# Optimization experiments

Measured on AMD Instinct MI355X. Metric: run time of the kernel, lower is better.

Reference implementation:

```python
import jax, jax.numpy as jnp
import numpy as np

B, T, C = 4, 2048, 1024
L = 256
H = 16
HS = C // H  # 64

def setup_inputs() -> dict:
    key = jax.random.key(0)
    ks = jax.random.split(key, 6)
    s = 0.02
    return {
        "x": jax.random.normal(ks[0], (B, T, C), dtype=jnp.float32),
        "Wq": jax.random.normal(ks[1], (C, C), dtype=jnp.float32) * s,
        "W_kv_down": jax.random.normal(ks[2], (C, L), dtype=jnp.float32) * s,
        "W_k_up": jax.random.normal(ks[3], (L, C), dtype=jnp.float32) * s,
        "W_v_up": jax.random.normal(ks[4], (L, C), dtype=jnp.float32) * s,
        "W_out": jax.random.normal(ks[5], (C, C), dtype=jnp.float32) * s,
    }

def reference(x, Wq, W_kv_down, W_k_up, W_v_up, W_out):
    # x: [B,T,C]
    q = (x @ Wq).reshape(B, T, H, HS).transpose(0, 2, 1, 3)        # [B,H,T,HS]
    latent_kv = x @ W_kv_down                                       # [B,T,L]
    k = (latent_kv @ W_k_up).reshape(B, T, H, HS).transpose(0, 2, 1, 3)
    v = (latent_kv @ W_v_up).reshape(B, T, H, HS).transpose(0, 2, 1, 3)
    att = jnp.einsum('bhtd,bhsd->bhts', q, k) / jnp.sqrt(jnp.float32(HS))
    causal = jnp.tril(jnp.ones((T, T), dtype=bool))
    att = jnp.where(causal[None, None], att, jnp.float32(-jnp.inf))
    att = jax.nn.softmax(att, axis=-1)
    y = jnp.einsum('bhts,bhsd->bhtd', att, v)                       # [B,H,T,HS]
    y = y.transpose(0, 2, 1, 3).reshape(B, T, C)
    return y @ W_out
```

## Files before the change

kernel.cpp:

```cpp
#include <hip/hip_runtime.h>
#include <cstddef>
#include <cstdint>

#define BB 4
#define TT 2048
#define CC 1024
#define LL 256
#define HH 16
#define DD 64
#define QLD (CC + LL)

typedef __attribute__((ext_vector_type(8))) short s16x8;
typedef __attribute__((ext_vector_type(4))) float f32x4;

static __device__ inline unsigned short f2bf(float f) {
    union { float f; unsigned u; } v; v.f = f;
    unsigned r = v.u + 0x7fffu + ((v.u >> 16) & 1u);
    return (unsigned short)(r >> 16);
}

static __device__ inline float fast_exp2(float x) {
#if __has_builtin(__builtin_amdgcn_exp2f)
    return __builtin_amdgcn_exp2f(x);
#else
    return exp2f(x);
#endif
}

static __device__ inline unsigned pack_bf16_trunc(float lo, float hi) {
    union { float f; unsigned u; } a, b;
    a.f = lo; b.f = hi;
    return __builtin_amdgcn_perm(b.u, a.u, 0x07060302u);
}

#define GLDS16(g, l)                                             \
    __builtin_amdgcn_global_load_lds(                            \
        (__attribute__((address_space(1))) void*)(g),            \
        (__attribute__((address_space(3))) void*)(l), 16, 0, 0)

extern "C" __global__ __launch_bounds__(256)
void fused_cvt(const float* __restrict__ x, unsigned short* __restrict__ xb,
               const float* __restrict__ Wq, const float* __restrict__ Wkv,
               const float* __restrict__ Wk, const float* __restrict__ Wv,
               const float* __restrict__ Wo,
               unsigned short* __restrict__ W1t, unsigned short* __restrict__ W2t,
               unsigned short* __restrict__ Wot, float qscale) {
    __shared__ unsigned short Ts[64][72];
    const int t = threadIdx.x;
    int blk = blockIdx.x;
    if (blk < 8192) {
        const int i = blk * 256 + t;
        const float4 v = ((const float4*)x)[i];
        ushort4 o;
        o.x = f2bf(v.x); o.y = f2bf(v.y); o.z = f2bf(v.z); o.w = f2bf(v.w);
        ((ushort4*)xb)[i] = o;
        return;
    }
    blk -= 8192;
    const float* W; unsigned short* Wt; int K, N; float scale; int tile;
    if (blk < 256)      { W = Wq;  Wt = W1t;                      K = CC; N = CC; scale = qscale; tile = blk; }
    else if (blk < 320) { W = Wkv; Wt = W1t + (size_t)CC * CC;    K = CC; N = LL; scale = 1.f;    tile = blk - 256; }
    else if (blk < 384) { W = Wk;  Wt = W2t;                      K = LL; N = CC; scale = 1.f;    tile = blk - 320; }
    else if (blk < 448) { W = Wv;  Wt = W2t + (size_t)CC * LL;    K = LL; N = CC; scale = 1.f;    tile = blk - 384; }
    else                { W = Wo;  Wt = Wot;                      K = CC; N = CC; scale = 1.f;    tile = blk - 448; }
    const int ktiles = K >> 6;
    const int k0 = (tile % ktiles) * 64, n0 = (tile / ktiles) * 64;
#pragma unroll
    for (int l = 0; l < 4; ++l) {
        const int idx = t + l * 256;
        const int r = idx >> 4, c4 = (idx & 15) * 4;
        const float4 v = *(const float4*)(W + (size_t)(k0 + r) * N + n0 + c4);
        Ts[c4 + 0][r] = f2bf(v.x * scale); Ts[c4 + 1][r] = f2bf(v.y * scale);
        Ts[c4 + 2][r] = f2bf(v.z * scale); Ts[c4 + 3][r] = f2bf(v.w * scale);
    }
    __syncthreads();
#pragma unroll
    for (int l = 0; l < 2; ++l) {
        const int idx = t + l * 256;
        const int n = idx >> 3, seg = idx & 7;
        *(s16x8*)(Wt + (size_t)(n0 + n) * K + k0 + seg * 8) = *(const s16x8*)&Ts[n][seg * 8];
    }
}

template <int MODE>
__global__ __launch_bounds__(256)
void bgemm(const unsigned short* __restrict__ A, const unsigned short* __restrict__ Bt,
           void* __restrict__ Cv, void* __restrict__ Cv2,
           int M, int N, int K, int lda, int ldc) {
    __shared__ unsigned short As[128][64];
    __shared__ unsigned short Bs[128][64];
    const int t = threadIdx.x;
    const int w = t >> 6, lane = t & 63, quad = lane >> 4, l16 = lane & 15;
    const int wm = w & 1, wn = w >> 1;

    int wg = blockIdx.y * gridDim.x + blockIdx.x;
    const int nwg = gridDim.x * gridDim.y;
    if ((nwg & 7) == 0) wg = (wg & 7) * (nwg >> 3) + (wg >> 3);
    const int bx = wg % gridDim.x, by = wg / gridDim.x;
    const int row0 = by * 128, col0 = bx * 128;

    const int sr = lane >> 3;
    const int sc = ((lane & 7) ^ sr) * 8;

    f32x4 acc[4][4];
#pragma unroll
    for (int i = 0; i < 4; ++i)
#pragma unroll
        for (int j = 0; j < 4; ++j) acc[i][j] = (f32x4){0.f, 0.f, 0.f, 0.f};

    const unsigned short* Ab = A + (size_t)(row0 + w * 32 + sr) * lda + sc;
    const unsigned short* Bb = Bt + (size_t)(col0 + w * 32 + sr) * K + sc;

    for (int k0 = 0; k0 < K; k0 += 64) {
#pragma unroll
        for (int c = 0; c < 4; ++c) {
            GLDS16(Ab + (size_t)(c * 8) * lda + k0, &As[w * 32 + c * 8][0]);
            GLDS16(Bb + (size_t)(c * 8) * K + k0, &Bs[w * 32 + c * 8][0]);
        }
        __syncthreads();
#pragma unroll
        for (int kk = 0; kk < 2; ++kk) {
            s16x8 af[4], bfr[4];
#pragma unroll
            for (int mt = 0; mt < 4; ++mt)
                af[mt] = *(const s16x8*)
                    &As[wm * 64 + mt * 16 + l16][((kk * 4 + quad) ^ (l16 & 7)) * 8];
#pragma unroll
            for (int nt = 0; nt < 4; ++nt)
                bfr[nt] = *(const s16x8*)
                    &Bs[wn * 64 + nt * 16 + l16][((kk * 4 + quad) ^ (l16 & 7)) * 8];
#pragma unroll
            for (int mt = 0; mt < 4; ++mt)
#pragma unroll
                for (int nt = 0; nt < 4; ++nt)
                    acc[mt][nt] = __builtin_amdgcn_mfma_f32_16x16x32_bf16(
                        af[mt], bfr[nt], acc[mt][nt], 0, 0, 0);
        }
        __syncthreads();
    }

    if constexpr (MODE == 0) {
        float* C = (float*)Cv;
#pragma unroll
        for (int mt = 0; mt < 4; ++mt)
#pragma unroll
            for (int nt = 0; nt < 4; ++nt)
#pragma unroll
                for (int r = 0; r < 4; ++r)
                    C[(size_t)(row0 + wm * 64 + mt * 16 + quad * 4 + r) * ldc +
                      col0 + wn * 64 + nt * 16 + l16] = acc[mt][nt][r];
    } else if constexpr (MODE == 1) {
        unsigned short* C = (unsigned short*)Cv;
#pragma unroll
        for (int mt = 0; mt < 4; ++mt)
#pragma unroll
            for (int nt = 0; nt < 4; ++nt)
#pragma unroll
                for (int r = 0; r < 4; ++r)
                    C[(size_t)(row0 + wm * 64 + mt * 16 + quad * 4 + r) * ldc +
                      col0 + wn * 64 + nt * 16 + l16] = f2bf(acc[mt][nt][r]);
    } else {
        if (col0 < CC) {
            unsigned short* C = (unsigned short*)Cv;
#pragma unroll
            for (int mt = 0; mt < 4; ++mt)
#pragma unroll
                for (int nt = 0; nt < 4; ++nt)
#pragma unroll
                    for (int r = 0; r < 4; ++r)
                        C[(size_t)(row0 + wm * 64 + mt * 16 + quad * 4 + r) * ldc +
                          col0 + wn * 64 + nt * 16 + l16] = f2bf(acc[mt][nt][r]);
        } else {
            __shared__ unsigned short Tb[64][136];
            unsigned short* vt = (unsigned short*)Cv2;
            const int b   = row0 >> 11;
            const int tl0 = row0 & 2047;
#pragma unroll
            for (int h = 0; h < 2; ++h) {
                if (wn == h) {
#pragma unroll
                    for (int mt = 0; mt < 4; ++mt)
#pragma unroll
                        for (int nt = 0; nt < 4; ++nt)
#pragma unroll
                            for (int r = 0; r < 4; ++r)
                                Tb[nt * 16 + l16][wm * 64 + mt * 16 + quad * 4 + r] =
                                    f2bf(acc[mt][nt][r]);
                }
                __syncthreads();
                const int head = ((col0 - CC) >> 6) + h;
#pragma unroll
                for (int l = 0; l < 4; ++l) {
                    const int idx = t + l * 256;
                    const int dv = idx >> 4, seg = idx & 15;
                    *(s16x8*)(vt + (((size_t)b * HH + head) * DD + dv) * TT + tl0 + seg * 8) =
                        *(const s16x8*)&Tb[dv][seg * 8];
                }
                __syncthreads();
            }
        }
    }
}

extern "C" __global__ __launch_bounds__(256, 4)
void mla_attn2(const unsigned short* __restrict__ q,
               const unsigned short* __restrict__ k,
               const unsigned short* __restrict__ vt,
               unsigned short* __restrict__ y) {
    __shared__ unsigned short Ks[2][64][64];
    __shared__ unsigned short Vs[2][64][64];

    {
        const unsigned bid = blockIdx.y * gridDim.x + blockIdx.x;
        const unsigned stag = (bid * 0x9E3779B1u) >> 30;
        for (unsigned i = 0; i < stag; ++i) __builtin_amdgcn_s_sleep(23);
    }

    const int bh = blockIdx.x;
    const int qt2 = (gridDim.y - 1) - blockIdx.y;
    const int b = bh >> 4, h = bh & 15;
    const int t0 = qt2 * 128;
    const int t = threadIdx.x;
    const int w = t >> 6, lane = t & 63, quad = lane >> 4, l16 = lane & 15;
    const int qw0 = t0 + w * 32;
    const int swz = ((lane & 7) ^ ((lane >> 3) & 7)) * 8;
    const int lrow = lane >> 3;

    const unsigned short* kb0 = k + ((size_t)b * TT) * CC + h * DD;
    const unsigned short* vb0 = vt + ((size_t)(b * HH + h)) * DD * TT;

    s16x8 qf[2][2];
#pragma unroll
    for (int qs = 0; qs < 2; ++qs)
#pragma unroll
        for (int kh = 0; kh < 2; ++kh)
            qf[qs][kh] = *(const s16x8*)(q + ((size_t)b * TT + qw0 + qs * 16 + l16) * QLD +
                                         h * DD + kh * 32 + quad * 8);

    f32x4 o[2][4];
    float lsum[2] = {0.f, 0.f};
#pragma unroll
    for (int qs = 0; qs < 2; ++qs)
#pragma unroll
        for (int nt = 0; nt < 4; ++nt) o[qs][nt] = (f32x4){0.f, 0.f, 0.f, 0.f};

    const int nkt = 2 * qt2 + 2;

#define STAGE_KV(kt_, bi_)                                                     \
    do {                                                                       \
        const int s0_ = (kt_) * 64;                                            \
        _Pragma("unroll")                                                      \
        for (int c = 0; c < 2; ++c) {                                          \
            const int g = w * 2 + c;                                           \
            const int row = g * 8 + lrow;                                      \
            GLDS16(kb0 + (size_t)(s0_ + row) * CC + swz, &Ks[bi_][g * 8][0]);  \
            GLDS16(vb0 + (size_t)row * TT + s0_ + swz, &Vs[bi_][g * 8][0]);    \
        }                                                                      \
    } while (0)

    STAGE_KV(0, 0);
    __syncthreads();

    for (int kt = 0; kt < nkt; ++kt) {
        const int cur = kt & 1;
        if (kt + 1 < nkt) STAGE_KV(kt + 1, cur ^ 1);

        const int s0 = kt * 64;
        if (s0 <= qw0 + 31) {
            const unsigned short (*Kc)[64] = Ks[cur];
            const unsigned short (*Vc)[64] = Vs[cur];
            f32x4 st[2][4];
#pragma unroll
            for (int nt = 0; nt < 4; ++nt) {
                const int key = nt * 16 + l16;
                const s16x8 kf0 = *(const s16x8*)&Kc[key][((0 + quad) ^ (l16 & 7)) * 8];
                const s16x8 kf1 = *(const s16x8*)&Kc[key][((4 + quad) ^ (l16 & 7)) * 8];
#pragma unroll
                for (int qs = 0; qs < 2; ++qs) {
                    f32x4 acc = (f32x4){0.f, 0.f, 0.f, 0.f};
                    acc = __builtin_amdgcn_mfma_f32_16x16x32_bf16(kf0, qf[qs][0], acc, 0, 0, 0);
                    acc = __builtin_amdgcn_mfma_f32_16x16x32_bf16(kf1, qf[qs][1], acc, 0, 0, 0);
                    st[qs][nt] = acc;
                }
            }

            const bool maskedTile = (s0 + 63 > qw0);
            s16x8 pf[2][2];
#pragma unroll
            for (int qs = 0; qs < 2; ++qs) {
                const int qidx = qw0 + qs * 16 + l16;
                unsigned pc[4][2];
                float tsum = 0.f;
#pragma unroll
                for (int nt = 0; nt < 4; ++nt) {
                    const int key0 = s0 + nt * 16 + quad * 4;
                    float p[4];
#pragma unroll
                    for (int r = 0; r < 4; ++r) {
                        float sv = st[qs][nt][r];
                        if (maskedTile && (key0 + r > qidx)) sv = -1e30f;
                        p[r] = fast_exp2(sv);
                    }
                    tsum += (p[0] + p[1]) + (p[2] + p[3]);
                    pc[nt][0] = pack_bf16_trunc(p[0], p[1]);
                    pc[nt][1] = pack_bf16_trunc(p[2], p[3]);
                }
                lsum[qs] += tsum;
#pragma unroll
                for (int kh = 0; kh < 2; ++kh) {
                    auto s0a = __builtin_amdgcn_permlane32_swap(
                        (int)pc[2 * kh + 0][0], (int)pc[2 * kh + 1][0], false, false);
                    auto w02 = __builtin_amdgcn_permlane16_swap(s0a[0], s0a[1], false, false);
                    auto s1a = __builtin_amdgcn_permlane32_swap(
                        (int)pc[2 * kh + 0][1], (int)pc[2 * kh + 1][1], false, false);
                    auto w13 = __builtin_amdgcn_permlane16_swap(s1a[0], s1a[1], false, false);
                    union { unsigned u[4]; s16x8 v; } fu;
                    fu.u[0] = (unsigned)w02[0];
                    fu.u[1] = (unsigned)w13[0];
                    fu.u[2] = (unsigned)w02[1];
                    fu.u[3] = (unsigned)w13[1];
                    pf[qs][kh] = fu.v;
                }
            }

#pragma unroll
            for (int nt = 0; nt < 4; ++nt) {
                const int dv = nt * 16 + l16;
                const s16x8 vf0 = *(const s16x8*)&Vc[dv][((0 + quad) ^ (l16 & 7)) * 8];
                const s16x8 vf1 = *(const s16x8*)&Vc[dv][((4 + quad) ^ (l16 & 7)) * 8];
#pragma unroll
                for (int qs = 0; qs < 2; ++qs) {
                    o[qs][nt] = __builtin_amdgcn_mfma_f32_16x16x32_bf16(pf[qs][0], vf0,
                                                                        o[qs][nt], 0, 0, 0);
                    o[qs][nt] = __builtin_amdgcn_mfma_f32_16x16x32_bf16(pf[qs][1], vf1,
                                                                        o[qs][nt], 0, 0, 0);
                }
            }
        }
        __syncthreads();
    }

    float lfull[2];
#pragma unroll
    for (int qs = 0; qs < 2; ++qs) {
        float s = lsum[qs];
        s += __shfl_xor(s, 16);
        s += __shfl_xor(s, 32);
        lfull[qs] = s;
    }

#pragma unroll
    for (int qs = 0; qs < 2; ++qs) {
#pragma unroll
        for (int r = 0; r < 4; ++r) {
            const float inv = 1.f / __shfl(lfull[qs], quad * 4 + r);
            unsigned short* yb = y + ((size_t)b * TT + qw0 + qs * 16 + quad * 4 + r) * CC +
                                 h * DD + l16;
#pragma unroll
            for (int nt = 0; nt < 4; ++nt)
                yb[nt * 16] = f2bf(o[qs][nt][r] * inv);
        }
    }
}

extern "C" void kernel_launch(void* const* d_in, const int* in_sizes, int n_in,
                              void* d_out, int out_size, void* d_ws, size_t ws_size,
                              hipStream_t stream) {
    const float* x   = (const float*)d_in[0];
    const float* Wq  = (const float*)d_in[1];
    const float* Wkv = (const float*)d_in[2];
    const float* Wk  = (const float*)d_in[3];
    const float* Wv  = (const float*)d_in[4];
    const float* Wo  = (const float*)d_in[5];
    float* out = (float*)d_out;

    const int M = BB * TT;
    unsigned short* p = (unsigned short*)d_ws;
    unsigned short* xb    = p; p += (size_t)M * CC;
    unsigned short* qlatb = p; p += (size_t)M * QLD;
    unsigned short* kb    = p; p += (size_t)M * CC;
    unsigned short* vtb   = p; p += (size_t)M * CC;
    unsigned short* yb    = p; p += (size_t)M * CC;
    unsigned short* W1t   = p; p += (size_t)QLD * CC;
    unsigned short* W2t   = p; p += (size_t)(2 * CC) * LL;
    unsigned short* Wot   = p; p += (size_t)CC * CC;

    const float qscale = 0.125f * 1.44269504f;

    fused_cvt<<<8896, 256, 0, stream>>>(x, xb, Wq, Wkv, Wk, Wv, Wo,
                                        W1t, W2t, Wot, qscale);
    bgemm<1><<<dim3(QLD / 128, M / 128), 256, 0, stream>>>(
        xb, W1t, qlatb, nullptr, M, QLD, CC, CC, QLD);
    bgemm<3><<<dim3(2 * CC / 128, M / 128), 256, 0, stream>>>(
        qlatb + CC, W2t, kb, vtb, M, 2 * CC, LL, QLD, CC);
    mla_attn2<<<dim3(BB * HH, TT / 128), 256, 0, stream>>>(qlatb, kb, vtb, yb);
    bgemm<0><<<dim3(CC / 128, M / 128), 256, 0, stream>>>(
        yb, Wot, out, nullptr, M, CC, CC, CC, CC);
}
```

Before: 227.6 us.

## Pair complementary causal query tiles per block for balanced attention work

The attention kernel now uses 128-thread blocks, each handling two 64-row query tiles (qt = 31-p and qt = p), so every block does roughly the same amount of causal work. Previously each block handled one 128-row tile with four waves, and the blocks' causal work varied widely. Each wave now stages twice as many K/V rows. The grid shrinks to 16 blocks per head, and each block runs its two tiles one after the other, so there is less parallelism per block and more load-issue work per thread.

```diff
diff --git a/kernel.cpp b/kernel.cpp
--- a/kernel.cpp
+++ b/kernel.cpp
@@ -202,8 +202,8 @@
     }
 }
 
-extern "C" __global__ __launch_bounds__(256, 4)
-void mla_attn2(const unsigned short* __restrict__ q,
+extern "C" __global__ __launch_bounds__(128, 2)
+void mla_attn4(const unsigned short* __restrict__ q,
                const unsigned short* __restrict__ k,
                const unsigned short* __restrict__ vt,
                unsigned short* __restrict__ y) {
@@ -217,148 +217,152 @@
     }
 
     const int bh = blockIdx.x;
-    const int qt2 = (gridDim.y - 1) - blockIdx.y;
     const int b = bh >> 4, h = bh & 15;
-    const int t0 = qt2 * 128;
     const int t = threadIdx.x;
     const int w = t >> 6, lane = t & 63, quad = lane >> 4, l16 = lane & 15;
-    const int qw0 = t0 + w * 32;
     const int swz = ((lane & 7) ^ ((lane >> 3) & 7)) * 8;
     const int lrow = lane >> 3;
+    const int p = blockIdx.y;
 
     const unsigned short* kb0 = k + ((size_t)b * TT) * CC + h * DD;
     const unsigned short* vb0 = vt + ((size_t)(b * HH + h)) * DD * TT;
 
-    s16x8 qf[2][2];
-#pragma unroll
-    for (int qs = 0; qs < 2; ++qs)
-#pragma unroll
-        for (int kh = 0; kh < 2; ++kh)
-            qf[qs][kh] = *(const s16x8*)(q + ((size_t)b * TT + qw0 + qs * 16 + l16) * QLD +
-                                         h * DD + kh * 32 + quad * 8);
-
-    f32x4 o[2][4];
-    float lsum[2] = {0.f, 0.f};
-#pragma unroll
-    for (int qs = 0; qs < 2; ++qs)
-#pragma unroll
-        for (int nt = 0; nt < 4; ++nt) o[qs][nt] = (f32x4){0.f, 0.f, 0.f, 0.f};
-
-    const int nkt = 2 * qt2 + 2;
-
-#define STAGE_KV(kt_, bi_)                                                     \
+#define STAGE_KV(s0_, bi_)                                                     \
     do {                                                                       \
-        const int s0_ = (kt_) * 64;                                            \
         _Pragma("unroll")                                                      \
-        for (int c = 0; c < 2; ++c) {                                          \
-            const int g = w * 2 + c;                                           \
+        for (int c = 0; c < 4; ++c) {                                          \
+            const int g = w * 4 + c;                                           \
             const int row = g * 8 + lrow;                                      \
-            GLDS16(kb0 + (size_t)(s0_ + row) * CC + swz, &Ks[bi_][g * 8][0]);  \
-            GLDS16(vb0 + (size_t)row * TT + s0_ + swz, &Vs[bi_][g * 8][0]);    \
+            GLDS16(kb0 + (size_t)((s0_) + row) * CC + swz, &Ks[bi_][g * 8][0]);\
+            GLDS16(vb0 + (size_t)row * TT + (s0_) + swz, &Vs[bi_][g * 8][0]);  \
         }                                                                      \
     } while (0)
 
-    STAGE_KV(0, 0);
-    __syncthreads();
-
-    for (int kt = 0; kt < nkt; ++kt) {
-        const int cur = kt & 1;
-        if (kt + 1 < nkt) STAGE_KV(kt + 1, cur ^ 1);
-
-        const int s0 = kt * 64;
-        if (s0 <= qw0 + 31) {
-            const unsigned short (*Kc)[64] = Ks[cur];
-            const unsigned short (*Vc)[64] = Vs[cur];
-            f32x4 st[2][4];
-#pragma unroll
-            for (int nt = 0; nt < 4; ++nt) {
-                const int key = nt * 16 + l16;
-                const s16x8 kf0 = *(const s16x8*)&Kc[key][((0 + quad) ^ (l16 & 7)) * 8];
-                const s16x8 kf1 = *(const s16x8*)&Kc[key][((4 + quad) ^ (l16 & 7)) * 8];
+#pragma unroll 1
+    for (int item = 0; item < 2; ++item) {
+        const int qt = item == 0 ? (31 - p) : p;
+        const int qw0 = qt * 64 + w * 32;
+
+        s16x8 qf[2][2];
+#pragma unroll
+        for (int qs = 0; qs < 2; ++qs)
+#pragma unroll
+            for (int kh = 0; kh < 2; ++kh)
+                qf[qs][kh] = *(const s16x8*)(q + ((size_t)b * TT + qw0 + qs * 16 + l16) * QLD +
+                                             h * DD + kh * 32 + quad * 8);
+
+        f32x4 o[2][4];
+        float lsum[2] = {0.f, 0.f};
+#pragma unroll
+        for (int qs = 0; qs < 2; ++qs)
+#pragma unroll
+            for (int nt = 0; nt < 4; ++nt) o[qs][nt] = (f32x4){0.f, 0.f, 0.f, 0.f};
+
+        const int nkt = qt + 1;
+
+        STAGE_KV(0, 0);
+        __syncthreads();
+
+#pragma unroll 1
+        for (int kt = 0; kt < nkt; ++kt) {
+            const int cur = kt & 1;
+            if (kt + 1 < nkt) STAGE_KV((kt + 1) * 64, cur ^ 1);
+
+            const int s0 = kt * 64;
+            if (s0 <= qw0 + 31) {
+                const unsigned short (*Kc)[64] = Ks[cur];
+                const unsigned short (*Vc)[64] = Vs[cur];
+                f32x4 st[2][4];
+#pragma unroll
+                for (int nt = 0; nt < 4; ++nt) {
+                    const int key = nt * 16 + l16;
+                    const s16x8 kf0 = *(const s16x8*)&Kc[key][((0 + quad) ^ (l16 & 7)) * 8];
+                    const s16x8 kf1 = *(const s16x8*)&Kc[key][((4 + quad) ^ (l16 & 7)) * 8];
+#pragma unroll
+                    for (int qs = 0; qs < 2; ++qs) {
+                        f32x4 acc = (f32x4){0.f, 0.f, 0.f, 0.f};
+                        acc = __builtin_amdgcn_mfma_f32_16x16x32_bf16(kf0, qf[qs][0], acc, 0, 0, 0);
+                        acc = __builtin_amdgcn_mfma_f32_16x16x32_bf16(kf1, qf[qs][1], acc, 0, 0, 0);
+                        st[qs][nt] = acc;
+                    }
+                }
+
+                const bool maskedTile = (s0 + 63 > qw0);
+                s16x8 pf[2][2];
 #pragma unroll
                 for (int qs = 0; qs < 2; ++qs) {
-                    f32x4 acc = (f32x4){0.f, 0.f, 0.f, 0.f};
-                    acc = __builtin_amdgcn_mfma_f32_16x16x32_bf16(kf0, qf[qs][0], acc, 0, 0, 0);
-                    acc = __builtin_amdgcn_mfma_f32_16x16x32_bf16(kf1, qf[qs][1], acc, 0, 0, 0);
-                    st[qs][nt] = acc;
+                    const int qidx = qw0 + qs * 16 + l16;
+                    unsigned pc[4][2];
+                    float tsum = 0.f;
+#pragma unroll
+                    for (int nt = 0; nt < 4; ++nt) {
+                        const int key0 = s0 + nt * 16 + quad * 4;
+                        float pv[4];
+#pragma unroll
+                        for (int r = 0; r < 4; ++r) {
+                            float sv = st[qs][nt][r];
+                            if (maskedTile && (key0 + r > qidx)) sv = -1e30f;
+                            pv[r] = fast_exp2(sv);
+                        }
+                        tsum += (pv[0] + pv[1]) + (pv[2] + pv[3]);
+                        pc[nt][0] = pack_bf16_trunc(pv[0], pv[1]);
+                        pc[nt][1] = pack_bf16_trunc(pv[2], pv[3]);
+                    }
+                    lsum[qs] += tsum;
+#pragma unroll
+                    for (int kh = 0; kh < 2; ++kh) {
+                        auto s0a = __builtin_amdgcn_permlane32_swap(
+                            (int)pc[2 * kh + 0][0], (int)pc[2 * kh + 1][0], false, false);
+                        auto w02 = __builtin_amdgcn_permlane16_swap(s0a[0], s0a[1], false, false);
+                        auto s1a = __builtin_amdgcn_permlane32_swap(
+                            (int)pc[2 * kh + 0][1], (int)pc[2 * kh + 1][1], false, false);
+                        auto w13 = __builtin_amdgcn_permlane16_swap(s1a[0], s1a[1], false, false);
+                        union { unsigned u[4]; s16x8 v; } fu;
+                        fu.u[0] = (unsigned)w02[0];
+                        fu.u[1] = (unsigned)w13[0];
+                        fu.u[2] = (unsigned)w02[1];
+                        fu.u[3] = (unsigned)w13[1];
+                        pf[qs][kh] = fu.v;
+                    }
+                }
+
+#pragma unroll
+                for (int nt = 0; nt < 4; ++nt) {
+                    const int dv = nt * 16 + l16;
+                    const s16x8 vf0 = *(const s16x8*)&Vc[dv][((0 + quad) ^ (l16 & 7)) * 8];
+                    const s16x8 vf1 = *(const s16x8*)&Vc[dv][((4 + quad) ^ (l16 & 7)) * 8];
+#pragma unroll
+                    for (int qs = 0; qs < 2; ++qs) {
+                        o[qs][nt] = __builtin_amdgcn_mfma_f32_16x16x32_bf16(pf[qs][0], vf0,
+                                                                            o[qs][nt], 0, 0, 0);
+                        o[qs][nt] = __builtin_amdgcn_mfma_f32_16x16x32_bf16(pf[qs][1], vf1,
+                                                                            o[qs][nt], 0, 0, 0);
+                    }
                 }
             }
-
-            const bool maskedTile = (s0 + 63 > qw0);
-            s16x8 pf[2][2];
-#pragma unroll
-            for (int qs = 0; qs < 2; ++qs) {
-                const int qidx = qw0 + qs * 16 + l16;
-                unsigned pc[4][2];
-                float tsum = 0.f;
-#pragma unroll
-                for (int nt = 0; nt < 4; ++nt) {
-                    const int key0 = s0 + nt * 16 + quad * 4;
-                    float p[4];
-#pragma unroll
-                    for (int r = 0; r < 4; ++r) {
-                        float sv = st[qs][nt][r];
-                        if (maskedTile && (key0 + r > qidx)) sv = -1e30f;
-                        p[r] = fast_exp2(sv);
-                    }
-                    tsum += (p[0] + p[1]) + (p[2] + p[3]);
-                    pc[nt][0] = pack_bf16_trunc(p[0], p[1]);
-                    pc[nt][1] = pack_bf16_trunc(p[2], p[3]);
-                }
-                lsum[qs] += tsum;
-#pragma unroll
-                for (int kh = 0; kh < 2; ++kh) {
-                    auto s0a = __builtin_amdgcn_permlane32_swap(
-                        (int)pc[2 * kh + 0][0], (int)pc[2 * kh + 1][0], false, false);
-                    auto w02 = __builtin_amdgcn_permlane16_swap(s0a[0], s0a[1], false, false);
-                    auto s1a = __builtin_amdgcn_permlane32_swap(
-                        (int)pc[2 * kh + 0][1], (int)pc[2 * kh + 1][1], false, false);
-                    auto w13 = __builtin_amdgcn_permlane16_swap(s1a[0], s1a[1], false, false);
-                    union { unsigned u[4]; s16x8 v; } fu;
-                    fu.u[0] = (unsigned)w02[0];
-                    fu.u[1] = (unsigned)w13[0];
-                    fu.u[2] = (unsigned)w02[1];
-                    fu.u[3] = (unsigned)w13[1];
-                    pf[qs][kh] = fu.v;
-                }
+            __syncthreads();
+        }
+
+        float lfull[2];
+#pragma unroll
+        for (int qs = 0; qs < 2; ++qs) {
+            float s = lsum[qs];
+            s += __shfl_xor(s, 16);
+            s += __shfl_xor(s, 32);
+            lfull[qs] = s;
+        }
+
+#pragma unroll
+        for (int qs = 0; qs < 2; ++qs) {
+#pragma unroll
+            for (int r = 0; r < 4; ++r) {
+                const float inv = 1.f / __shfl(lfull[qs], quad * 4 + r);
+                unsigned short* yb = y + ((size_t)b * TT + qw0 + qs * 16 + quad * 4 + r) * CC +
+                                     h * DD + l16;
+#pragma unroll
+                for (int nt = 0; nt < 4; ++nt)
+                    yb[nt * 16] = f2bf(o[qs][nt][r] * inv);
             }
-
-#pragma unroll
-            for (int nt = 0; nt < 4; ++nt) {
-                const int dv = nt * 16 + l16;
-                const s16x8 vf0 = *(const s16x8*)&Vc[dv][((0 + quad) ^ (l16 & 7)) * 8];
-                const s16x8 vf1 = *(const s16x8*)&Vc[dv][((4 + quad) ^ (l16 & 7)) * 8];
-#pragma unroll
-                for (int qs = 0; qs < 2; ++qs) {
-                    o[qs][nt] = __builtin_amdgcn_mfma_f32_16x16x32_bf16(pf[qs][0], vf0,
-                                                                        o[qs][nt], 0, 0, 0);
-                    o[qs][nt] = __builtin_amdgcn_mfma_f32_16x16x32_bf16(pf[qs][1], vf1,
-                                                                        o[qs][nt], 0, 0, 0);
-                }
-            }
-        }
-        __syncthreads();
-    }
-
-    float lfull[2];
-#pragma unroll
-    for (int qs = 0; qs < 2; ++qs) {
-        float s = lsum[qs];
-        s += __shfl_xor(s, 16);
-        s += __shfl_xor(s, 32);
-        lfull[qs] = s;
-    }
-
-#pragma unroll
-    for (int qs = 0; qs < 2; ++qs) {
-#pragma unroll
-        for (int r = 0; r < 4; ++r) {
-            const float inv = 1.f / __shfl(lfull[qs], quad * 4 + r);
-            unsigned short* yb = y + ((size_t)b * TT + qw0 + qs * 16 + quad * 4 + r) * CC +
-                                 h * DD + l16;
-#pragma unroll
-            for (int nt = 0; nt < 4; ++nt)
-                yb[nt * 16] = f2bf(o[qs][nt][r] * inv);
         }
     }
 }
@@ -393,7 +397,7 @@
         xb, W1t, qlatb, nullptr, M, QLD, CC, CC, QLD);
     bgemm<3><<<dim3(2 * CC / 128, M / 128), 256, 0, stream>>>(
         qlatb + CC, W2t, kb, vtb, M, 2 * CC, LL, QLD, CC);
-    mla_attn2<<<dim3(BB * HH, TT / 128), 256, 0, stream>>>(qlatb, kb, vtb, yb);
+    mla_attn4<<<dim3(BB * HH, 16), 128, 0, stream>>>(qlatb, kb, vtb, yb);
     bgemm<0><<<dim3(CC / 128, M / 128), 256, 0, stream>>>(
         yb, Wot, out, nullptr, M, CC, CC, CC, CC);
 }
```

New measurement: 242.1 us. +6.4%, slower.

## Drop K/V double buffering in attention kernel and raise occupancy hint

Applied to the files above, without the earlier changes.

Removes the double-buffered shared-memory staging of K and V tiles in the attention kernel and uses a single buffer that is loaded and then synchronized each iteration. The launch bounds hint moves from 4 to 8 blocks per SM, halving LDS use per block so more waves can be resident. In exchange, the prefetch overlap of the next tile with compute is lost, and each tile load is now exposed, to be hidden only by the extra occupancy.

```diff
diff --git a/kernel.cpp b/kernel.cpp
--- a/kernel.cpp
+++ b/kernel.cpp
@@ -202,13 +202,13 @@
     }
 }
 
-extern "C" __global__ __launch_bounds__(256, 4)
+extern "C" __global__ __launch_bounds__(256, 8)
 void mla_attn2(const unsigned short* __restrict__ q,
                const unsigned short* __restrict__ k,
                const unsigned short* __restrict__ vt,
                unsigned short* __restrict__ y) {
-    __shared__ unsigned short Ks[2][64][64];
-    __shared__ unsigned short Vs[2][64][64];
+    __shared__ unsigned short Ks[64][64];
+    __shared__ unsigned short Vs[64][64];
 
     {
         const unsigned bid = blockIdx.y * gridDim.x + blockIdx.x;
@@ -246,35 +246,24 @@
 
     const int nkt = 2 * qt2 + 2;
 
-#define STAGE_KV(kt_, bi_)                                                     \
-    do {                                                                       \
-        const int s0_ = (kt_) * 64;                                            \
-        _Pragma("unroll")                                                      \
-        for (int c = 0; c < 2; ++c) {                                          \
-            const int g = w * 2 + c;                                           \
-            const int row = g * 8 + lrow;                                      \
-            GLDS16(kb0 + (size_t)(s0_ + row) * CC + swz, &Ks[bi_][g * 8][0]);  \
-            GLDS16(vb0 + (size_t)row * TT + s0_ + swz, &Vs[bi_][g * 8][0]);    \
-        }                                                                      \
-    } while (0)
-
-    STAGE_KV(0, 0);
-    __syncthreads();
-
     for (int kt = 0; kt < nkt; ++kt) {
-        const int cur = kt & 1;
-        if (kt + 1 < nkt) STAGE_KV(kt + 1, cur ^ 1);
-
         const int s0 = kt * 64;
+#pragma unroll
+        for (int c = 0; c < 2; ++c) {
+            const int g = w * 2 + c;
+            const int row = g * 8 + lrow;
+            GLDS16(kb0 + (size_t)(s0 + row) * CC + swz, &Ks[g * 8][0]);
+            GLDS16(vb0 + (size_t)row * TT + s0 + swz, &Vs[g * 8][0]);
+        }
+        __syncthreads();
+
         if (s0 <= qw0 + 31) {
-            const unsigned short (*Kc)[64] = Ks[cur];
-            const unsigned short (*Vc)[64] = Vs[cur];
             f32x4 st[2][4];
 #pragma unroll
             for (int nt = 0; nt < 4; ++nt) {
                 const int key = nt * 16 + l16;
-                const s16x8 kf0 = *(const s16x8*)&Kc[key][((0 + quad) ^ (l16 & 7)) * 8];
-                const s16x8 kf1 = *(const s16x8*)&Kc[key][((4 + quad) ^ (l16 & 7)) * 8];
+                const s16x8 kf0 = *(const s16x8*)&Ks[key][((0 + quad) ^ (l16 & 7)) * 8];
+                const s16x8 kf1 = *(const s16x8*)&Ks[key][((4 + quad) ^ (l16 & 7)) * 8];
 #pragma unroll
                 for (int qs = 0; qs < 2; ++qs) {
                     f32x4 acc = (f32x4){0.f, 0.f, 0.f, 0.f};
@@ -326,8 +315,8 @@
 #pragma unroll
             for (int nt = 0; nt < 4; ++nt) {
                 const int dv = nt * 16 + l16;
-                const s16x8 vf0 = *(const s16x8*)&Vc[dv][((0 + quad) ^ (l16 & 7)) * 8];
-                const s16x8 vf1 = *(const s16x8*)&Vc[dv][((4 + quad) ^ (l16 & 7)) * 8];
+                const s16x8 vf0 = *(const s16x8*)&Vs[dv][((0 + quad) ^ (l16 & 7)) * 8];
+                const s16x8 vf1 = *(const s16x8*)&Vs[dv][((4 + quad) ^ (l16 & 7)) * 8];
 #pragma unroll
                 for (int qs = 0; qs < 2; ++qs) {
                     o[qs][nt] = __builtin_amdgcn_mfma_f32_16x16x32_bf16(pf[qs][0], vf0,
```

Measured after the change: 574.1 us. 152% more time.

## Split attention query tile across eight waves of 16 rows each

Applied to the files above, without the earlier changes.

The attention kernel now launches 512 threads per block, so each of eight waves handles 16 query rows instead of four waves handling 32. The K/V staging is redistributed so that each wave loads one 8-row group. The goal is to cut per-wave register pressure and increase the number of resident waves to hide latency. The trade-off is that each K/V fragment read from LDS is reused by only one query subtile, which doubles LDS read traffic per unit of MFMA work and adds more waves contending at each barrier.

```diff
diff --git a/kernel.cpp b/kernel.cpp
--- a/kernel.cpp
+++ b/kernel.cpp
@@ -202,7 +202,7 @@
     }
 }
 
-extern "C" __global__ __launch_bounds__(256, 4)
+extern "C" __global__ __launch_bounds__(512, 6)
 void mla_attn2(const unsigned short* __restrict__ q,
                const unsigned short* __restrict__ k,
                const unsigned short* __restrict__ vt,
@@ -222,40 +222,32 @@
     const int t0 = qt2 * 128;
     const int t = threadIdx.x;
     const int w = t >> 6, lane = t & 63, quad = lane >> 4, l16 = lane & 15;
-    const int qw0 = t0 + w * 32;
+    const int qw0 = t0 + w * 16;
     const int swz = ((lane & 7) ^ ((lane >> 3) & 7)) * 8;
     const int lrow = lane >> 3;
 
     const unsigned short* kb0 = k + ((size_t)b * TT) * CC + h * DD;
     const unsigned short* vb0 = vt + ((size_t)(b * HH + h)) * DD * TT;
 
-    s16x8 qf[2][2];
-#pragma unroll
-    for (int qs = 0; qs < 2; ++qs)
-#pragma unroll
-        for (int kh = 0; kh < 2; ++kh)
-            qf[qs][kh] = *(const s16x8*)(q + ((size_t)b * TT + qw0 + qs * 16 + l16) * QLD +
-                                         h * DD + kh * 32 + quad * 8);
-
-    f32x4 o[2][4];
-    float lsum[2] = {0.f, 0.f};
-#pragma unroll
-    for (int qs = 0; qs < 2; ++qs)
-#pragma unroll
-        for (int nt = 0; nt < 4; ++nt) o[qs][nt] = (f32x4){0.f, 0.f, 0.f, 0.f};
+    s16x8 qf[2];
+#pragma unroll
+    for (int kh = 0; kh < 2; ++kh)
+        qf[kh] = *(const s16x8*)(q + ((size_t)b * TT + qw0 + l16) * QLD +
+                                 h * DD + kh * 32 + quad * 8);
+
+    f32x4 o[4];
+    float lsum = 0.f;
+#pragma unroll
+    for (int nt = 0; nt < 4; ++nt) o[nt] = (f32x4){0.f, 0.f, 0.f, 0.f};
 
     const int nkt = 2 * qt2 + 2;
 
 #define STAGE_KV(kt_, bi_)                                                     \
     do {                                                                       \
         const int s0_ = (kt_) * 64;                                            \
-        _Pragma("unroll")                                                      \
-        for (int c = 0; c < 2; ++c) {                                          \
-            const int g = w * 2 + c;                                           \
-            const int row = g * 8 + lrow;                                      \
-            GLDS16(kb0 + (size_t)(s0_ + row) * CC + swz, &Ks[bi_][g * 8][0]);  \
-            GLDS16(vb0 + (size_t)row * TT + s0_ + swz, &Vs[bi_][g * 8][0]);    \
-        }                                                                      \
+        const int row = w * 8 + lrow;                                          \
+        GLDS16(kb0 + (size_t)(s0_ + row) * CC + swz, &Ks[bi_][w * 8][0]);      \
+        GLDS16(vb0 + (size_t)row * TT + s0_ + swz, &Vs[bi_][w * 8][0]);        \
     } while (0)
 
     STAGE_KV(0, 0);
@@ -266,61 +258,55 @@
         if (kt + 1 < nkt) STAGE_KV(kt + 1, cur ^ 1);
 
         const int s0 = kt * 64;
-        if (s0 <= qw0 + 31) {
+        if (s0 <= qw0 + 15) {
             const unsigned short (*Kc)[64] = Ks[cur];
             const unsigned short (*Vc)[64] = Vs[cur];
-            f32x4 st[2][4];
+            f32x4 st[4];
 #pragma unroll
             for (int nt = 0; nt < 4; ++nt) {
                 const int key = nt * 16 + l16;
                 const s16x8 kf0 = *(const s16x8*)&Kc[key][((0 + quad) ^ (l16 & 7)) * 8];
                 const s16x8 kf1 = *(const s16x8*)&Kc[key][((4 + quad) ^ (l16 & 7)) * 8];
-#pragma unroll
-                for (int qs = 0; qs < 2; ++qs) {
-                    f32x4 acc = (f32x4){0.f, 0.f, 0.f, 0.f};
-                    acc = __builtin_amdgcn_mfma_f32_16x16x32_bf16(kf0, qf[qs][0], acc, 0, 0, 0);
-                    acc = __builtin_amdgcn_mfma_f32_16x16x32_bf16(kf1, qf[qs][1], acc, 0, 0, 0);
-                    st[qs][nt] = acc;
+                f32x4 acc = (f32x4){0.f, 0.f, 0.f, 0.f};
+                acc = __builtin_amdgcn_mfma_f32_16x16x32_bf16(kf0, qf[0], acc, 0, 0, 0);
+                acc = __builtin_amdgcn_mfma_f32_16x16x32_bf16(kf1, qf[1], acc, 0, 0, 0);
+                st[nt] = acc;
+            }
+
+            const bool maskedTile = (s0 + 63 > qw0);
+            const int qidx = qw0 + l16;
+            unsigned pc[4][2];
+            float tsum = 0.f;
+#pragma unroll
+            for (int nt = 0; nt < 4; ++nt) {
+                const int key0 = s0 + nt * 16 + quad * 4;
+                float p[4];
+#pragma unroll
+                for (int r = 0; r < 4; ++r) {
+                    float sv = st[nt][r];
+                    if (maskedTile && (key0 + r > qidx)) sv = -1e30f;
+                    p[r] = fast_exp2(sv);
                 }
-            }
-
-            const bool maskedTile = (s0 + 63 > qw0);
-            s16x8 pf[2][2];
-#pragma unroll
-            for (int qs = 0; qs < 2; ++qs) {
-                const int qidx = qw0 + qs * 16 + l16;
-                unsigned pc[4][2];
-                float tsum = 0.f;
-#pragma unroll
-                for (int nt = 0; nt < 4; ++nt) {
-                    const int key0 = s0 + nt * 16 + quad * 4;
-                    float p[4];
-#pragma unroll
-                    for (int r = 0; r < 4; ++r) {
-                        float sv = st[qs][nt][r];
-                        if (maskedTile && (key0 + r > qidx)) sv = -1e30f;
-                        p[r] = fast_exp2(sv);
-                    }
-                    tsum += (p[0] + p[1]) + (p[2] + p[3]);
-                    pc[nt][0] = pack_bf16_trunc(p[0], p[1]);
-                    pc[nt][1] = pack_bf16_trunc(p[2], p[3]);
-                }
-                lsum[qs] += tsum;
-#pragma unroll
-                for (int kh = 0; kh < 2; ++kh) {
-                    auto s0a = __builtin_amdgcn_permlane32_swap(
-                        (int)pc[2 * kh + 0][0], (int)pc[2 * kh + 1][0], false, false);
-                    auto w02 = __builtin_amdgcn_permlane16_swap(s0a[0], s0a[1], false, false);
-                    auto s1a = __builtin_amdgcn_permlane32_swap(
-                        (int)pc[2 * kh + 0][1], (int)pc[2 * kh + 1][1], false, false);
-                    auto w13 = __builtin_amdgcn_permlane16_swap(s1a[0], s1a[1], false, false);
-                    union { unsigned u[4]; s16x8 v; } fu;
-                    fu.u[0] = (unsigned)w02[0];
-                    fu.u[1] = (unsigned)w13[0];
-                    fu.u[2] = (unsigned)w02[1];
-                    fu.u[3] = (unsigned)w13[1];
-                    pf[qs][kh] = fu.v;
-                }
+                tsum += (p[0] + p[1]) + (p[2] + p[3]);
+                pc[nt][0] = pack_bf16_trunc(p[0], p[1]);
+                pc[nt][1] = pack_bf16_trunc(p[2], p[3]);
+            }
+            lsum += tsum;
+            s16x8 pf[2];
+#pragma unroll
+            for (int kh = 0; kh < 2; ++kh) {
+                auto s0a = __builtin_amdgcn_permlane32_swap(
+                    (int)pc[2 * kh + 0][0], (int)pc[2 * kh + 1][0], false, false);
+                auto w02 = __builtin_amdgcn_permlane16_swap(s0a[0], s0a[1], false, false);
+                auto s1a = __builtin_amdgcn_permlane32_swap(
+                    (int)pc[2 * kh + 0][1], (int)pc[2 * kh + 1][1], false, false);
+                auto w13 = __builtin_amdgcn_permlane16_swap(s1a[0], s1a[1], false, false);
+                union { unsigned u[4]; s16x8 v; } fu;
+                fu.u[0] = (unsigned)w02[0];
+                fu.u[1] = (unsigned)w13[0];
+                fu.u[2] = (unsigned)w02[1];
+                fu.u[3] = (unsigned)w13[1];
+                pf[kh] = fu.v;
             }
 
 #pragma unroll
@@ -328,38 +314,25 @@
                 const int dv = nt * 16 + l16;
                 const s16x8 vf0 = *(const s16x8*)&Vc[dv][((0 + quad) ^ (l16 & 7)) * 8];
                 const s16x8 vf1 = *(const s16x8*)&Vc[dv][((4 + quad) ^ (l16 & 7)) * 8];
-#pragma unroll
-                for (int qs = 0; qs < 2; ++qs) {
-                    o[qs][nt] = __builtin_amdgcn_mfma_f32_16x16x32_bf16(pf[qs][0], vf0,
-                                                                        o[qs][nt], 0, 0, 0);
-                    o[qs][nt] = __builtin_amdgcn_mfma_f32_16x16x32_bf16(pf[qs][1], vf1,
-                                                                        o[qs][nt], 0, 0, 0);
-                }
+                o[nt] = __builtin_amdgcn_mfma_f32_16x16x32_bf16(pf[0], vf0, o[nt], 0, 0, 0);
+                o[nt] = __builtin_amdgcn_mfma_f32_16x16x32_bf16(pf[1], vf1, o[nt], 0, 0, 0);
             }
         }
         __syncthreads();
     }
 
-    float lfull[2];
-#pragma unroll
-    for (int qs = 0; qs < 2; ++qs) {
-        float s = lsum[qs];
-        s += __shfl_xor(s, 16);
-        s += __shfl_xor(s, 32);
-        lfull[qs] = s;
-    }
-
-#pragma unroll
-    for (int qs = 0; qs < 2; ++qs) {
-#pragma unroll
-        for (int r = 0; r < 4; ++r) {
-            const float inv = 1.f / __shfl(lfull[qs], quad * 4 + r);
-            unsigned short* yb = y + ((size_t)b * TT + qw0 + qs * 16 + quad * 4 + r) * CC +
-                                 h * DD + l16;
-#pragma unroll
-            for (int nt = 0; nt < 4; ++nt)
-                yb[nt * 16] = f2bf(o[qs][nt][r] * inv);
-        }
+    float lfull = lsum;
+    lfull += __shfl_xor(lfull, 16);
+    lfull += __shfl_xor(lfull, 32);
+
+#pragma unroll
+    for (int r = 0; r < 4; ++r) {
+        const float inv = 1.f / __shfl(lfull, quad * 4 + r);
+        unsigned short* yb = y + ((size_t)b * TT + qw0 + quad * 4 + r) * CC +
+                             h * DD + l16;
+#pragma unroll
+        for (int nt = 0; nt < 4; ++nt)
+            yb[nt * 16] = f2bf(o[nt][r] * inv);
     }
 }
 
@@ -393,7 +366,7 @@
         xb, W1t, qlatb, nullptr, M, QLD, CC, CC, QLD);
     bgemm<3><<<dim3(2 * CC / 128, M / 128), 256, 0, stream>>>(
         qlatb + CC, W2t, kb, vtb, M, 2 * CC, LL, QLD, CC);
-    mla_attn2<<<dim3(BB * HH, TT / 128), 256, 0, stream>>>(qlatb, kb, vtb, yb);
+    mla_attn2<<<dim3(BB * HH, TT / 128), 512, 0, stream>>>(qlatb, kb, vtb, yb);
     bgemm<0><<<dim3(CC / 128, M / 128), 256, 0, stream>>>(
         yb, Wot, out, nullptr, M, CC, CC, CC, CC);
 }
```

Result: no change. 223.9 us (-1.6%).
